# Kernel tuning notes

Measured on AMD Instinct MI355X. Metric: run time of the kernel, lower is better.

Reference implementation:

```python
import jax, jax.numpy as jnp
import numpy as np

C_M, C_Z, C_H = 256, 128, 32
EPS = 1e-3
LN_EPS = 1e-5


def setup_inputs() -> dict:
    key = jax.random.key(0)
    ks = jax.random.split(key, 10)
    S, R = 128, 256
    inp = {
        'm_1': jax.random.normal(ks[0], (S, R, C_M), jnp.float32),
        'm_2': jax.random.normal(ks[1], (S, R, C_M), jnp.float32),
        'mask_1': jnp.ones((S, R), jnp.float32),
        'mask_2': jnp.ones((S, R), jnp.float32),
        # LayerNorm params
        'ln1_w': jnp.ones((C_M,), jnp.float32),
        'ln1_b': jnp.zeros((C_M,), jnp.float32),
        'ln2_w': jnp.ones((C_M,), jnp.float32),
        'ln2_b': jnp.zeros((C_M,), jnp.float32),
        # Linear params
        'w1': jax.random.normal(ks[2], (C_M, C_H), jnp.float32) * (1.0 / np.sqrt(C_M)),
        'b1': jnp.zeros((C_H,), jnp.float32),
        'w2': jax.random.normal(ks[3], (C_M, C_H), jnp.float32) * (1.0 / np.sqrt(C_M)),
        'b2': jnp.zeros((C_H,), jnp.float32),
        'w_out': jax.random.normal(ks[4], (C_H * C_H, C_Z), jnp.float32) * 0.02,
        'b_out': jnp.zeros((C_Z,), jnp.float32),
    }
    return inp


def _layer_norm(x, w, b):
    mu = jnp.mean(x, axis=-1, keepdims=True)
    var = jnp.mean(jnp.square(x - mu), axis=-1, keepdims=True)
    return (x - mu) * jax.lax.rsqrt(var + LN_EPS) * w + b


def reference(m_1, m_2, mask_1, mask_2, ln1_w, ln1_b, ln2_w, ln2_b,
              w1, b1, w2, b2, w_out, b_out):
    # m_*: [S, R, C_M]; mask_*: [S, R]
    a = (_layer_norm(m_1, ln1_w, ln1_b) @ w1 + b1) * mask_1[..., None]  # [S,R,H]
    b = (_layer_norm(m_2, ln2_w, ln2_b) @ w2 + b2) * mask_2[..., None]  # [S,R,H]
    # outer product mean over sequence dim: [R, R, H, H]
    outer = jnp.einsum('sic,sje->ijce', a, b)
    S, R, H = a.shape
    outer = outer.reshape(R, R, H * H)
    z = outer @ w_out + b_out  # [R, R, C_Z]
    norm = jnp.einsum('si,sj->ij', mask_1, mask_2)[..., None] + EPS  # [R,R,1]
    return z / norm
```

## Files before the change

kernel.cpp:

```cpp
#include <hip/hip_runtime.h>
#include <hip/hip_bf16.h>

#define S_DIM 128
#define R_DIM 256
#define CM    256
#define H_DIM 32
#define CZ    128

typedef short s8v   __attribute__((ext_vector_type(8)));
typedef float f32x4 __attribute__((ext_vector_type(4)));
typedef float f32x16 __attribute__((ext_vector_type(16)));
using bf16 = __hip_bfloat16;

static __device__ __forceinline__ unsigned short bf16_bits(float f) {
  return __builtin_bit_cast(unsigned short, __float2bfloat16(f));
}

static __device__ __forceinline__ void gload_lds16(const void* g, void* l) {
  __builtin_amdgcn_global_load_lds(
      (const __attribute__((address_space(1))) unsigned int*)g,
      (__attribute__((address_space(3))) unsigned int*)l, 16, 0, 0);
}

__global__ __launch_bounds__(256) void opm_prep(
    const float* __restrict__ w_out,
    const float* __restrict__ mask1, const float* __restrict__ mask2,
    const float* __restrict__ w1, const float* __restrict__ w2,
    bf16* __restrict__ wT2, float* __restrict__ rnorm, bf16* __restrict__ wF)
{
  const int b   = blockIdx.x;
  const int tid = threadIdx.x;
  if (b < 64) {
    const int vid  = b*256 + tid;
    const int lane = vid & 63;
    const int ks2  = (vid >> 6) & 63;
    const int tb   = vid >> 12;
    const int t    = tb*32 + (lane & 31);
    const int hf   = lane >> 5;
    unsigned int pk[4];
    #pragma unroll
    for (int ep = 0; ep < 4; ++ep) {
      const int ce0 = ks2*16 + hf*8 + ep*2;
      const int ce1 = ce0 + 1;
      unsigned int w0 = bf16_bits(w_out[((ce0 & 31)*32 + (ce0 >> 5))*CZ + t]);
      unsigned int w1b = bf16_bits(w_out[((ce1 & 31)*32 + (ce1 >> 5))*CZ + t]);
      pk[ep] = w0 | (w1b << 16);
    }
    uint4 o = {pk[0], pk[1], pk[2], pk[3]};
    *reinterpret_cast<uint4*>((char*)wT2 + (size_t)vid*16) = o;
  } else if (b < 320) {
    const int i = b - 64;
    const int j = tid;
    float acc = 0.f;
    for (int s = 0; s < S_DIM; ++s)
      acc += mask1[(size_t)s*R_DIM + i] * mask2[(size_t)s*R_DIM + j];
    rnorm[i*R_DIM + j] = 1.0f / (acc + 1e-3f);
  } else {
    const int mat = b - 320;
    const float* __restrict__ w = mat ? w2 : w1;
    bf16* __restrict__ dst = wF + mat*8192;
    #pragma unroll
    for (int it = 0; it < 4; ++it) {
      const int vid  = it*256 + tid;
      const int nf   = vid >> 9;
      const int ks   = (vid >> 6) & 7;
      const int lane = vid & 63;
      const int h    = nf*16 + (lane & 15);
      unsigned int pk[4];
      #pragma unroll
      for (int ep = 0; ep < 4; ++ep) {
        const int c0 = ks*32 + (lane >> 4)*8 + ep*2;
        unsigned int lo = bf16_bits(w[c0*H_DIM + h]);
        unsigned int hi = bf16_bits(w[(c0 + 1)*H_DIM + h]);
        pk[ep] = lo | (hi << 16);
      }
      uint4 o = {pk[0], pk[1], pk[2], pk[3]};
      *reinterpret_cast<uint4*>((char*)dst + (size_t)vid*16) = o;
    }
  }
}

__global__ __launch_bounds__(64) void opm_proj(
    const float* __restrict__ m1, const float* __restrict__ m2,
    const float* __restrict__ ln1w, const float* __restrict__ ln1b,
    const float* __restrict__ ln2w, const float* __restrict__ ln2b,
    const float* __restrict__ b1, const float* __restrict__ b2,
    const float* __restrict__ mask1, const float* __restrict__ mask2,
    const bf16* __restrict__ wF, bf16* __restrict__ aT, bf16* __restrict__ bT)
{
  __shared__ char xn[8192];

  const int mat = blockIdx.y;
  const float* __restrict__ m    = mat ? m2   : m1;
  const float* __restrict__ lnw  = mat ? ln2w : ln1w;
  const float* __restrict__ lnb  = mat ? ln2b : ln1b;
  const float* __restrict__ bias = mat ? b2   : b1;
  const float* __restrict__ mask = mat ? mask2 : mask1;
  const bf16* __restrict__ wf    = wF + mat*8192;
  bf16* __restrict__ dst         = mat ? bT   : aT;

  const int lane = threadIdx.x;
  const int row  = lane & 15;
  const int q    = lane >> 4;
  const int r    = blockIdx.x & 255;
  const int sb   = blockIdx.x >> 8;
  const int s    = sb*16 + row;

  const float4* __restrict__ src =
      reinterpret_cast<const float4*>(m + ((size_t)s*R_DIM + r)*CM + q*64);
  float4 x[16];
  float sum = 0.f, sq = 0.f;
  #pragma unroll
  for (int i = 0; i < 16; ++i) {
    x[i] = src[i];
    sum += x[i].x + x[i].y + x[i].z + x[i].w;
    sq  += x[i].x*x[i].x + x[i].y*x[i].y + x[i].z*x[i].z + x[i].w*x[i].w;
  }
  sum += __shfl_xor(sum, 16); sum += __shfl_xor(sum, 32);
  sq  += __shfl_xor(sq, 16);  sq  += __shfl_xor(sq, 32);
  const float mu = sum * (1.0f/CM);
  const float rs = rsqrtf(sq * (1.0f/CM) - mu*mu + 1e-5f);

  const float4* __restrict__ lw4 = reinterpret_cast<const float4*>(lnw + q*64);
  const float4* __restrict__ lb4 = reinterpret_cast<const float4*>(lnb + q*64);
  #pragma unroll
  for (int i2 = 0; i2 < 8; ++i2) {
    unsigned int pk[4];
    #pragma unroll
    for (int half = 0; half < 2; ++half) {
      const int i = i2*2 + half;
      const float4 lw = lw4[i];
      const float4 lb = lb4[i];
      const float v0 = (x[i].x - mu)*rs*lw.x + lb.x;
      const float v1 = (x[i].y - mu)*rs*lw.y + lb.y;
      const float v2 = (x[i].z - mu)*rs*lw.z + lb.z;
      const float v3 = (x[i].w - mu)*rs*lw.w + lb.w;
      pk[half*2+0] = (unsigned)bf16_bits(v0) | ((unsigned)bf16_bits(v1) << 16);
      pk[half*2+1] = (unsigned)bf16_bits(v2) | ((unsigned)bf16_bits(v3) << 16);
    }
    int off = row*512 + q*128 + i2*16;
    off ^= (row & 7) << 4;
    uint4 o = {pk[0], pk[1], pk[2], pk[3]};
    *reinterpret_cast<uint4*>(xn + off) = o;
  }
  __syncthreads();

  const float bv0 = bias[row];
  const float bv1 = bias[16 + row];
  f32x4 z0 = {bv0, bv0, bv0, bv0};
  f32x4 z1 = {bv1, bv1, bv1, bv1};
  #pragma unroll
  for (int ks = 0; ks < 8; ++ks) {
    int off = row*512 + ks*64 + q*16;
    off ^= (row & 7) << 4;
    const s8v a  = *reinterpret_cast<const s8v*>(xn + off);
    const s8v w0 = *reinterpret_cast<const s8v*>((const char*)wf + (ks*64 + lane)*16);
    const s8v w1 = *reinterpret_cast<const s8v*>((const char*)wf + ((8 + ks)*64 + lane)*16);
    z0 = __builtin_amdgcn_mfma_f32_16x16x32_bf16(a, w0, z0, 0, 0, 0);
    z1 = __builtin_amdgcn_mfma_f32_16x16x32_bf16(a, w1, z1, 0, 0, 0);
  }

  float mk[4];
  #pragma unroll
  for (int rr = 0; rr < 4; ++rr)
    mk[rr] = mask[(size_t)(sb*16 + q*4 + rr)*R_DIM + r];

  unsigned int pa0 = (unsigned)bf16_bits(z0[0]*mk[0]) | ((unsigned)bf16_bits(z0[1]*mk[1]) << 16);
  unsigned int pa1 = (unsigned)bf16_bits(z0[2]*mk[2]) | ((unsigned)bf16_bits(z0[3]*mk[3]) << 16);
  unsigned int pb0 = (unsigned)bf16_bits(z1[0]*mk[0]) | ((unsigned)bf16_bits(z1[1]*mk[1]) << 16);
  unsigned int pb1 = (unsigned)bf16_bits(z1[2]*mk[2]) | ((unsigned)bf16_bits(z1[3]*mk[3]) << 16);

  const int p0 = r*H_DIM + row;
  const int p1 = r*H_DIM + 16 + row;
  const int c0 = sb*2 + (q >> 1);
  const int rem = (q & 1) * 8;
  {
    uint2 v; v.x = pa0; v.y = pa1;
    *reinterpret_cast<uint2*>((char*)dst + (size_t)p0*256 + ((c0 ^ (p0 & 15)) << 4) + rem) = v;
  }
  {
    uint2 v; v.x = pb0; v.y = pb1;
    *reinterpret_cast<uint2*>((char*)dst + (size_t)p1*256 + ((c0 ^ (p1 & 15)) << 4) + rem) = v;
  }
}

__global__ __launch_bounds__(1024, 4) void opm_gemm(
    const bf16* __restrict__ aT, const bf16* __restrict__ bT,
    const bf16* __restrict__ wT2, const float* __restrict__ b_out,
    const float* __restrict__ rnorm, float* __restrict__ out)
{
  __shared__ char smem[131072];

  const int tid  = threadIdx.x;
  const int lane = tid & 63;
  const int wid  = tid >> 6;
  const int l31  = lane & 31;
  const int hf   = lane >> 5;

  int swz = blockIdx.x;
  swz = (swz & 7)*128 + (swz >> 3);
  const int bx = swz >> 5, by = swz & 31;

  {
    const char* gA = (const char*)aT + (size_t)bx*65536;
    const char* gB = (const char*)bT + (size_t)by*65536;
    #pragma unroll
    for (int i = 0; i < 4; ++i) {
      const int base = (i*16 + wid)*1024;
      gload_lds16(gA + base + lane*16, smem + base);
      gload_lds16(gB + base + lane*16, smem + 65536 + base);
    }
  }
  __syncthreads();

  const int wm = wid >> 2, wn = wid & 3;
  f32x16 acc[2][2];
  #pragma unroll
  for (int mf = 0; mf < 2; ++mf)
    #pragma unroll
    for (int nf = 0; nf < 2; ++nf)
      #pragma unroll
      for (int r = 0; r < 16; ++r) acc[mf][nf][r] = 0.f;

  #pragma unroll
  for (int ks = 0; ks < 8; ++ks) {
    s8v af[2], bfv[2];
    #pragma unroll
    for (int mf = 0; mf < 2; ++mf) {
      const int mm = wm*64 + mf*32 + l31;
      int L = (mm*256 + ks*32 + hf*16) ^ ((mm & 15) << 4);
      af[mf] = *reinterpret_cast<const s8v*>(smem + L);
    }
    #pragma unroll
    for (int nf = 0; nf < 2; ++nf) {
      const int nn = wn*64 + nf*32 + l31;
      int L = (nn*256 + ks*32 + hf*16) ^ ((nn & 15) << 4);
      bfv[nf] = *reinterpret_cast<const s8v*>(smem + 65536 + L);
    }
    #pragma unroll
    for (int mf = 0; mf < 2; ++mf)
      #pragma unroll
      for (int nf = 0; nf < 2; ++nf)
        acc[mf][nf] = __builtin_amdgcn_mfma_f32_32x32x16_bf16(af[mf], bfv[nf], acc[mf][nf], 0, 0, 0);
  }
  __syncthreads();

  #pragma unroll
  for (int mf = 0; mf < 2; ++mf) {
    #pragma unroll
    for (int nf = 0; nf < 2; ++nf) {
      const int pair = (wm*2 + mf)*8 + wn*2 + nf;
      #pragma unroll
      for (int g = 0; g < 4; ++g) {
        const unsigned int lo = (unsigned)bf16_bits(acc[mf][nf][4*g+0]) |
                                ((unsigned)bf16_bits(acc[mf][nf][4*g+1]) << 16);
        const unsigned int hi = (unsigned)bf16_bits(acc[mf][nf][4*g+2]) |
                                ((unsigned)bf16_bits(acc[mf][nf][4*g+3]) << 16);
        const int L0 = pair*2048 + (l31*32 + 8*g + 4*hf)*2;
        const int L  = L0 ^ ((((pair & 15) ^ ((L0 >> 7) & 15))) << 4);
        uint2 v; v.x = lo; v.y = hi;
        *reinterpret_cast<uint2*>(smem + L) = v;
      }
    }
  }
  __syncthreads();

  const int kq = wid >> 2, pn = wid & 3;
  const int t  = pn*32 + l31;
  f32x16 z0, z1;
  {
    const float init = (kq == 0) ? b_out[t] : 0.f;
    #pragma unroll
    for (int r = 0; r < 16; ++r) { z0[r] = init; z1[r] = init; }
  }
  {
    const char* wb = (const char*)wT2 + ((size_t)(pn*64 + kq*16)*64 + lane)*16;
    #pragma unroll
    for (int ks = 0; ks < 16; ++ks) {
      const int ks2 = kq*16 + ks;
      const s8v bw = *reinterpret_cast<const s8v*>(wb + ks*1024);
      {
        const int pair = l31;
        int L0 = pair*2048 + ks2*32 + hf*16;
        int L  = L0 ^ ((((pair & 15) ^ ((L0 >> 7) & 15))) << 4);
        const s8v a = *reinterpret_cast<const s8v*>(smem + L);
        z0 = __builtin_amdgcn_mfma_f32_32x32x16_bf16(a, bw, z0, 0, 0, 0);
      }
      {
        const int pair = 32 + l31;
        int L0 = pair*2048 + ks2*32 + hf*16;
        int L  = L0 ^ ((((pair & 15) ^ ((L0 >> 7) & 15))) << 4);
        const s8v a = *reinterpret_cast<const s8v*>(smem + L);
        z1 = __builtin_amdgcn_mfma_f32_32x32x16_bf16(a, bw, z1, 0, 0, 0);
      }
    }
  }
  __syncthreads();

  if (kq != 0) {
    const int base = (kq - 1)*32768 + pn*8192;
    #pragma unroll
    for (int g = 0; g < 4; ++g) {
      f32x4 v0 = {z0[4*g+0], z0[4*g+1], z0[4*g+2], z0[4*g+3]};
      f32x4 v1 = {z1[4*g+0], z1[4*g+1], z1[4*g+2], z1[4*g+3]};
      *reinterpret_cast<f32x4*>(smem + base +        g*1024 + lane*16) = v0;
      *reinterpret_cast<f32x4*>(smem + base + 4096 + g*1024 + lane*16) = v1;
    }
  }
  __syncthreads();

  if (kq == 0) {
    #pragma unroll
    for (int g = 0; g < 4; ++g) {
      #pragma unroll
      for (int kk = 0; kk < 3; ++kk) {
        const int base = kk*32768 + pn*8192;
        const f32x4 p0 = *reinterpret_cast<const f32x4*>(smem + base +        g*1024 + lane*16);
        const f32x4 p1 = *reinterpret_cast<const f32x4*>(smem + base + 4096 + g*1024 + lane*16);
        #pragma unroll
        for (int j = 0; j < 4; ++j) { z0[4*g+j] += p0[j]; z1[4*g+j] += p1[j]; }
      }
    }
    #pragma unroll
    for (int r = 0; r < 16; ++r) {
      const int row = (r & 3) + 8*(r >> 2) + 4*hf;
      {
        const int pr = row;
        const int o  = (bx*8 + (pr >> 3))*R_DIM + by*8 + (pr & 7);
        out[(size_t)o*CZ + t] = z0[r] * rnorm[o];
      }
      {
        const int pr = 32 + row;
        const int o  = (bx*8 + (pr >> 3))*R_DIM + by*8 + (pr & 7);
        out[(size_t)o*CZ + t] = z1[r] * rnorm[o];
      }
    }
  }
}

extern "C" void kernel_launch(void* const* d_in, const int* in_sizes, int n_in,
                              void* d_out, int out_size, void* d_ws, size_t ws_size,
                              hipStream_t stream) {
  const float* m_1    = (const float*)d_in[0];
  const float* m_2    = (const float*)d_in[1];
  const float* mask_1 = (const float*)d_in[2];
  const float* mask_2 = (const float*)d_in[3];
  const float* ln1_w  = (const float*)d_in[4];
  const float* ln1_b  = (const float*)d_in[5];
  const float* ln2_w  = (const float*)d_in[6];
  const float* ln2_b  = (const float*)d_in[7];
  const float* w1     = (const float*)d_in[8];
  const float* b1     = (const float*)d_in[9];
  const float* w2     = (const float*)d_in[10];
  const float* b2     = (const float*)d_in[11];
  const float* w_out  = (const float*)d_in[12];
  const float* b_out  = (const float*)d_in[13];
  float* out = (float*)d_out;

  char* ws = (char*)d_ws;
  bf16* aT    = (bf16*)ws;
  bf16* bT    = (bf16*)(ws + (2u << 20));
  bf16* wT2   = (bf16*)(ws + (4u << 20));
  float* rnrm = (float*)(ws + (4u << 20) + (256u << 10));
  bf16* wF    = (bf16*)(ws + (4u << 20) + (512u << 10));

  opm_prep<<<dim3(322),      dim3(256), 0, stream>>>(w_out, mask_1, mask_2,
      w1, w2, wT2, rnrm, wF);
  opm_proj<<<dim3(2048, 2),  dim3(64),  0, stream>>>(m_1, m_2, ln1_w, ln1_b,
      ln2_w, ln2_b, b1, b2, mask_1, mask_2, wF, aT, bT);
  opm_gemm<<<dim3(1024),     dim3(1024), 0, stream>>>(aT, bT, wT2, b_out, rnrm, out);
}
```

Measured before the change: 75.91 us.

## Prefetch w_out fragments into registers and distribute split-K reduction across all waves

```diff
diff --git a/kernel.cpp b/kernel.cpp
--- a/kernel.cpp
+++ b/kernel.cpp
@@ -245,60 +245,80 @@
   }
   __syncthreads();
 
-  #pragma unroll
-  for (int mf = 0; mf < 2; ++mf) {
-    #pragma unroll
-    for (int nf = 0; nf < 2; ++nf) {
-      const int pair = (wm*2 + mf)*8 + wn*2 + nf;
-      #pragma unroll
-      for (int g = 0; g < 4; ++g) {
-        const unsigned int lo = (unsigned)bf16_bits(acc[mf][nf][4*g+0]) |
-                                ((unsigned)bf16_bits(acc[mf][nf][4*g+1]) << 16);
-        const unsigned int hi = (unsigned)bf16_bits(acc[mf][nf][4*g+2]) |
-                                ((unsigned)bf16_bits(acc[mf][nf][4*g+3]) << 16);
-        const int L0 = pair*2048 + (l31*32 + 8*g + 4*hf)*2;
-        const int L  = L0 ^ ((((pair & 15) ^ ((L0 >> 7) & 15))) << 4);
-        uint2 v; v.x = lo; v.y = hi;
-        *reinterpret_cast<uint2*>(smem + L) = v;
-      }
-    }
-  }
-  __syncthreads();
-
-  const int kq = wid >> 2, pn = wid & 3;
-  const int t  = pn*32 + l31;
+  const int kq = wm, pn = wn;
+  const char* wb = (const char*)wT2 + ((size_t)(pn*64 + kq*16)*64 + lane)*16;
+  s8v bwr[16];
+
+  #pragma unroll
+  for (int i = 0; i < 8; ++i)
+    bwr[i] = *reinterpret_cast<const s8v*>(wb + i*1024);
+
+  #pragma unroll
+  for (int nf = 0; nf < 2; ++nf) {
+    const int pair = (wm*2 + 0)*8 + wn*2 + nf;
+    #pragma unroll
+    for (int g = 0; g < 4; ++g) {
+      const unsigned int lo = (unsigned)bf16_bits(acc[0][nf][4*g+0]) |
+                              ((unsigned)bf16_bits(acc[0][nf][4*g+1]) << 16);
+      const unsigned int hi = (unsigned)bf16_bits(acc[0][nf][4*g+2]) |
+                              ((unsigned)bf16_bits(acc[0][nf][4*g+3]) << 16);
+      const int L0 = pair*2048 + (l31*32 + 8*g + 4*hf)*2;
+      const int L  = L0 ^ ((((pair & 15) ^ ((L0 >> 7) & 15))) << 4);
+      uint2 v; v.x = lo; v.y = hi;
+      *reinterpret_cast<uint2*>(smem + L) = v;
+    }
+  }
+
+  #pragma unroll
+  for (int i = 8; i < 16; ++i)
+    bwr[i] = *reinterpret_cast<const s8v*>(wb + i*1024);
+
+  #pragma unroll
+  for (int nf = 0; nf < 2; ++nf) {
+    const int pair = (wm*2 + 1)*8 + wn*2 + nf;
+    #pragma unroll
+    for (int g = 0; g < 4; ++g) {
+      const unsigned int lo = (unsigned)bf16_bits(acc[1][nf][4*g+0]) |
+                              ((unsigned)bf16_bits(acc[1][nf][4*g+1]) << 16);
+      const unsigned int hi = (unsigned)bf16_bits(acc[1][nf][4*g+2]) |
+                              ((unsigned)bf16_bits(acc[1][nf][4*g+3]) << 16);
+      const int L0 = pair*2048 + (l31*32 + 8*g + 4*hf)*2;
+      const int L  = L0 ^ ((((pair & 15) ^ ((L0 >> 7) & 15))) << 4);
+      uint2 v; v.x = lo; v.y = hi;
+      *reinterpret_cast<uint2*>(smem + L) = v;
+    }
+  }
+  __syncthreads();
+
+  const int t = pn*32 + l31;
   f32x16 z0, z1;
   {
     const float init = (kq == 0) ? b_out[t] : 0.f;
     #pragma unroll
     for (int r = 0; r < 16; ++r) { z0[r] = init; z1[r] = init; }
   }
-  {
-    const char* wb = (const char*)wT2 + ((size_t)(pn*64 + kq*16)*64 + lane)*16;
-    #pragma unroll
-    for (int ks = 0; ks < 16; ++ks) {
-      const int ks2 = kq*16 + ks;
-      const s8v bw = *reinterpret_cast<const s8v*>(wb + ks*1024);
-      {
-        const int pair = l31;
-        int L0 = pair*2048 + ks2*32 + hf*16;
-        int L  = L0 ^ ((((pair & 15) ^ ((L0 >> 7) & 15))) << 4);
-        const s8v a = *reinterpret_cast<const s8v*>(smem + L);
-        z0 = __builtin_amdgcn_mfma_f32_32x32x16_bf16(a, bw, z0, 0, 0, 0);
-      }
-      {
-        const int pair = 32 + l31;
-        int L0 = pair*2048 + ks2*32 + hf*16;
-        int L  = L0 ^ ((((pair & 15) ^ ((L0 >> 7) & 15))) << 4);
-        const s8v a = *reinterpret_cast<const s8v*>(smem + L);
-        z1 = __builtin_amdgcn_mfma_f32_32x32x16_bf16(a, bw, z1, 0, 0, 0);
-      }
-    }
-  }
-  __syncthreads();
-
-  if (kq != 0) {
-    const int base = (kq - 1)*32768 + pn*8192;
+  #pragma unroll
+  for (int ks = 0; ks < 16; ++ks) {
+    const int ks2 = kq*16 + ks;
+    {
+      const int pair = l31;
+      int L0 = pair*2048 + ks2*32 + hf*16;
+      int L  = L0 ^ ((((pair & 15) ^ ((L0 >> 7) & 15))) << 4);
+      const s8v a = *reinterpret_cast<const s8v*>(smem + L);
+      z0 = __builtin_amdgcn_mfma_f32_32x32x16_bf16(a, bwr[ks], z0, 0, 0, 0);
+    }
+    {
+      const int pair = 32 + l31;
+      int L0 = pair*2048 + ks2*32 + hf*16;
+      int L  = L0 ^ ((((pair & 15) ^ ((L0 >> 7) & 15))) << 4);
+      const s8v a = *reinterpret_cast<const s8v*>(smem + L);
+      z1 = __builtin_amdgcn_mfma_f32_32x32x16_bf16(a, bwr[ks], z1, 0, 0, 0);
+    }
+  }
+  __syncthreads();
+
+  {
+    const int base = wid*8192;
     #pragma unroll
     for (int g = 0; g < 4; ++g) {
       f32x4 v0 = {z0[4*g+0], z0[4*g+1], z0[4*g+2], z0[4*g+3]};
@@ -309,30 +329,32 @@
   }
   __syncthreads();
 
-  if (kq == 0) {
-    #pragma unroll
-    for (int g = 0; g < 4; ++g) {
-      #pragma unroll
-      for (int kk = 0; kk < 3; ++kk) {
-        const int base = kk*32768 + pn*8192;
-        const f32x4 p0 = *reinterpret_cast<const f32x4*>(smem + base +        g*1024 + lane*16);
-        const f32x4 p1 = *reinterpret_cast<const f32x4*>(smem + base + 4096 + g*1024 + lane*16);
+  {
+    const int chain = kq & 1;
+    const int gh    = kq >> 1;
+    f32x4 f[2];
+    #pragma unroll
+    for (int gg = 0; gg < 2; ++gg) {
+      const int g = gh*2 + gg;
+      f32x4 s = {0.f, 0.f, 0.f, 0.f};
+      #pragma unroll
+      for (int kk = 0; kk < 4; ++kk) {
+        const int base = (kk*4 + pn)*8192 + chain*4096;
+        const f32x4 p = *reinterpret_cast<const f32x4*>(smem + base + g*1024 + lane*16);
         #pragma unroll
-        for (int j = 0; j < 4; ++j) { z0[4*g+j] += p0[j]; z1[4*g+j] += p1[j]; }
+        for (int j = 0; j < 4; ++j) s[j] += p[j];
       }
-    }
-    #pragma unroll
-    for (int r = 0; r < 16; ++r) {
-      const int row = (r & 3) + 8*(r >> 2) + 4*hf;
-      {
-        const int pr = row;
-        const int o  = (bx*8 + (pr >> 3))*R_DIM + by*8 + (pr & 7);
-        out[(size_t)o*CZ + t] = z0[r] * rnorm[o];
-      }
-      {
-        const int pr = 32 + row;
-        const int o  = (bx*8 + (pr >> 3))*R_DIM + by*8 + (pr & 7);
-        out[(size_t)o*CZ + t] = z1[r] * rnorm[o];
+      f[gg] = s;
+    }
+    #pragma unroll
+    for (int gg = 0; gg < 2; ++gg) {
+      const int g = gh*2 + gg;
+      #pragma unroll
+      for (int j = 0; j < 4; ++j) {
+        const int row  = j + 4*hf + 8*g;
+        const int pair = chain*32 + row;
+        const int o    = (bx*8 + (pair >> 3))*R_DIM + by*8 + (pair & 7);
+        out[(size_t)o*CZ + t] = f[gg][j] * rnorm[o];
       }
     }
   }
```

New measurement: 77.13 us. About the same (+1.6%).
